# Optimization experiments

Measured on AMD Instinct MI355X. Metric: run time of the kernel, lower is better.

Reference implementation:

```python
import jax, jax.numpy as jnp
import numpy as np

B, T, H, L = 64, 64, 256, 2
INPUT_SIZE = 65
E = INPUT_SIZE - 1  # encoder_in


def setup_inputs() -> dict:
    key = jax.random.key(0)
    ks = jax.random.split(key, 20)
    s = 0.05
    p = {}
    p["input_data"] = jax.random.normal(ks[0], (B, T, INPUT_SIZE), jnp.float32)
    # encoder LSTM (input E -> H, L layers; torch gate order i,f,g,o)
    p["w_ih_e0"] = jax.random.normal(ks[1], (4 * H, E), jnp.float32) * s
    p["w_ih_e1"] = jax.random.normal(ks[2], (L - 1, 4 * H, H), jnp.float32) * s
    p["w_hh_e"] = jax.random.normal(ks[3], (L, 4 * H, H), jnp.float32) * s
    p["b_ih_e"] = jax.random.normal(ks[4], (L, 4 * H), jnp.float32) * s
    p["b_hh_e"] = jax.random.normal(ks[5], (L, 4 * H), jnp.float32) * s
    # decoder LSTM (input H+1 -> H, L layers)
    p["w_ih_d0"] = jax.random.normal(ks[6], (4 * H, H + 1), jnp.float32) * s
    p["w_ih_d1"] = jax.random.normal(ks[7], (L - 1, 4 * H, H), jnp.float32) * s
    p["w_hh_d"] = jax.random.normal(ks[8], (L, 4 * H, H), jnp.float32) * s
    p["b_ih_d"] = jax.random.normal(ks[9], (L, 4 * H), jnp.float32) * s
    p["b_hh_d"] = jax.random.normal(ks[10], (L, 4 * H), jnp.float32) * s
    # encoder attention MLP: Linear(2H+T -> E), Tanh, Linear(E -> 1, no bias)
    p["attn_w1"] = jax.random.normal(ks[11], (E, 2 * H + T), jnp.float32) * s
    p["attn_b1"] = jax.random.normal(ks[12], (E,), jnp.float32) * s
    p["attn_w2"] = jax.random.normal(ks[13], (E,), jnp.float32) * s
    # decoder attention MLP: Linear(3H -> H), Tanh, Linear(H -> 1, no bias)
    p["attnd_w1"] = jax.random.normal(ks[14], (H, 3 * H), jnp.float32) * s
    p["attnd_b1"] = jax.random.normal(ks[15], (H,), jnp.float32) * s
    p["attnd_w2"] = jax.random.normal(ks[16], (H,), jnp.float32) * s
    # output projection: Linear(2H -> 1)
    p["proj_w"] = jax.random.normal(ks[17], (1, 2 * H), jnp.float32) * s
    p["proj_b"] = jax.random.normal(ks[18], (1,), jnp.float32) * s
    return p


def _lstm_step(x, h, c, w_ih0, w_ih_rest, w_hh, b_ih, b_hh):
    """Single-timestep multi-layer LSTM. x: [B, in], h/c: [L, B, H]."""
    hs, cs = [], []
    inp = x
    for l in range(L):
        w_ih = w_ih0 if l == 0 else w_ih_rest[l - 1]
        gates = inp @ w_ih.T + b_ih[l] + h[l] @ w_hh[l].T + b_hh[l]  # [B, 4H]
        i, f, g, o = jnp.split(gates, 4, axis=-1)
        c_new = jax.nn.sigmoid(f) * c[l] + jax.nn.sigmoid(i) * jnp.tanh(g)
        h_new = jax.nn.sigmoid(o) * jnp.tanh(c_new)
        hs.append(h_new)
        cs.append(c_new)
        inp = h_new
    return jnp.stack(hs), jnp.stack(cs)


def reference(input_data, w_ih_e0, w_ih_e1, w_hh_e, b_ih_e, b_hh_e,
              w_ih_d0, w_ih_d1, w_hh_d, b_ih_d, b_hh_d,
              attn_w1, attn_b1, attn_w2, attnd_w1, attnd_b1, attnd_w2,
              proj_w, proj_b):
    input_encoder = input_data[:, :, 1:]             # [B, T, E]
    input_decoder = input_data[:, :, 0]              # [B, T]
    input_permuted = jnp.transpose(input_encoder, (0, 2, 1))  # [B, E, T]

    h0 = jnp.zeros((L, B, H), input_data.dtype)
    c0 = jnp.zeros((L, B, H), input_data.dtype)

    def enc_step(carry, x_t):  # x_t: [B, E]
        h, c = carry
        feat = jnp.concatenate([
            jnp.broadcast_to(h[-1][:, None, :], (B, E, H)),
            jnp.broadcast_to(c[-1][:, None, :], (B, E, H)),
            input_permuted], axis=-1)                # [B, E, 2H+T]
        z = jnp.tanh(feat @ attn_w1.T + attn_b1)     # [B, E, E]
        a = jax.nn.softmax(z @ attn_w2, axis=-1)     # [B, E]
        h, c = _lstm_step(x_t * a, h, c, w_ih_e0, w_ih_e1, w_hh_e, b_ih_e, b_hh_e)
        return (h, c), h[-1]

    _, h_tops = jax.lax.scan(enc_step, (h0, c0), jnp.transpose(input_encoder, (1, 0, 2)))
    h_expanded = jnp.transpose(h_tops, (1, 0, 2))    # [B, T, H]

    def dec_step(carry, d_t):  # d_t: [B]
        h, c = carry
        feat = jnp.concatenate([
            jnp.broadcast_to(h[-1][:, None, :], (B, T, H)),
            jnp.broadcast_to(c[-1][:, None, :], (B, T, H)),
            h_expanded], axis=-1)                    # [B, T, 3H]
        z = jnp.tanh(feat @ attnd_w1.T + attnd_b1)   # [B, T, H]
        a = jax.nn.softmax(z @ attnd_w2, axis=-1)    # [B, T]
        partial = jnp.einsum('bth,bt->bh', h_expanded, a)  # [B, H]
        full = jnp.concatenate([partial, d_t[:, None]], axis=-1)  # [B, H+1]
        h, c = _lstm_step(full, h, c, w_ih_d0, w_ih_d1, w_hh_d, b_ih_d, b_hh_d)
        return (h, c), partial

    (h_d, c_d), partials = jax.lax.scan(dec_step, (h0, c0), input_decoder.T)
    out = jnp.abs(jnp.concatenate([h_d[-1], partials[-1]], axis=-1) @ proj_w.T + proj_b)  # [B, 1]
    return out
```

## Files before the change

### kernel.cpp

```cpp
#include <hip/hip_runtime.h>
#include <hip/hip_fp16.h>
#include <math.h>

#define NT8 512
#define NT  1024

typedef _Float16 h2v __attribute__((ext_vector_type(2)));
union H8 { uint4 u; h2v h[4]; };

__device__ __forceinline__ float sigf(float x)   { return 1.0f / (1.0f + __expf(-x)); }
__device__ __forceinline__ float tanhf_(float x) { return 1.0f - 2.0f / (1.0f + __expf(2.0f * x)); }
__device__ __forceinline__ float dot4(float4 a, float4 b) {
    return a.x * b.x + a.y * b.y + a.z * b.z + a.w * b.w;
}
__device__ __forceinline__ float red16(float v) {
    v += __shfl_xor(v, 1); v += __shfl_xor(v, 2);
    v += __shfl_xor(v, 4); v += __shfl_xor(v, 8);
    return v;
}
__device__ __forceinline__ float red8(float v) {
    v += __shfl_xor(v, 1); v += __shfl_xor(v, 2); v += __shfl_xor(v, 4);
    return v;
}
__device__ __forceinline__ float red64(float v) {
    v += __shfl_xor(v, 1);  v += __shfl_xor(v, 2);  v += __shfl_xor(v, 4);
    v += __shfl_xor(v, 8);  v += __shfl_xor(v, 16); v += __shfl_xor(v, 32);
    return v;
}
__device__ __forceinline__ float dot2h(h2v a, h2v b, float c) {
#if __has_builtin(__builtin_amdgcn_fdot2)
    return __builtin_amdgcn_fdot2(a, b, c, false);
#else
    return c + (float)a[0] * (float)b[0] + (float)a[1] * (float)b[1];
#endif
}

__device__ __forceinline__ float exr(const float* p) {
    return __hip_atomic_load(p, __ATOMIC_RELAXED, __HIP_MEMORY_SCOPE_AGENT);
}
__device__ __forceinline__ void xsig(unsigned* ctr) {
    if (threadIdx.x == 0) {
        asm volatile("s_waitcnt vmcnt(0)" ::: "memory");
        __hip_atomic_fetch_add(ctr, 1u, __ATOMIC_RELAXED, __HIP_MEMORY_SCOPE_AGENT);
    }
}
__device__ __forceinline__ void xwait(unsigned* ctr, unsigned target) {
    if (threadIdx.x == 0) {
        while (__hip_atomic_load(ctr, __ATOMIC_RELAXED, __HIP_MEMORY_SCOPE_AGENT) < target)
            __builtin_amdgcn_s_sleep(1);
    }
    __syncthreads();
}

#define OFF_RA   0
#define OFF_RE0  32768
#define OFF_RE1  425984
#define OFF_RDW1 950272
#define OFF_RD0  1081344
#define OFF_RDT  1605632
#define OFF_RD1  1606656
#define OFF_RPD  2130944
#define TOT_H2   2196480

template<int ITERS, bool BIAS, bool DT>
__device__ __forceinline__ void gemvS512(const __half* __restrict__ W,
                                         const __half* __restrict__ act,
                                         const float* __restrict__ biasF,
                                         const __half* __restrict__ rdtH, float dts,
                                         float* __restrict__ outg, int coB) {
    const int lane = threadIdx.x & 63;
    const int q = lane & 15, g = lane >> 4;
    const int w = threadIdx.x >> 6;
    H8 a0, a1, a2, a3;
    a0.u = *(const uint4*)(act + 8 * q);
    a1.u = *(const uint4*)(act + 8 * q + 128);
    a2.u = *(const uint4*)(act + 8 * q + 256);
    a3.u = *(const uint4*)(act + 8 * q + 384);
    #pragma unroll 2
    for (int it = 0; it < ITERS; ++it) {
        const int l = w * 16 + it * 4 + g;
        const int j = ((l & 0x60) << 3) + coB + (l & 31);
        const uint4* wp = (const uint4*)(W + ((size_t)j << 9) + 32 * q);
        H8 w0, w1, w2, w3;
        w0.u = wp[0]; w1.u = wp[1]; w2.u = wp[2]; w3.u = wp[3];
        float s0 = 0.f, s1 = 0.f;
        #pragma unroll
        for (int i = 0; i < 4; ++i) {
            s0 = dot2h(w0.h[i], a0.h[i], s0);
            s1 = dot2h(w1.h[i], a1.h[i], s1);
            s0 = dot2h(w2.h[i], a2.h[i], s0);
            s1 = dot2h(w3.h[i], a3.h[i], s1);
        }
        float s = red16(s0 + s1);
        if (q == 0) {
            if (DT) s += dts * (float)rdtH[l];
            outg[l] = BIAS ? s + biasF[l] : s;
        }
    }
}

template<int ITERS>
__device__ __forceinline__ void gemvS384(const __half* __restrict__ W,
                                         const __half* __restrict__ act,
                                         const float* __restrict__ biasF,
                                         float* __restrict__ outg, int coB) {
    const int lane = threadIdx.x & 63;
    const int q = lane & 15, g = lane >> 4;
    const int w = threadIdx.x >> 6;
    H8 a0, a1, a2;
    a0.u = *(const uint4*)(act + 8 * q);
    a1.u = *(const uint4*)(act + 8 * q + 128);
    a2.u = *(const uint4*)(act + 8 * q + 256);
    #pragma unroll 2
    for (int it = 0; it < ITERS; ++it) {
        const int l = w * 16 + it * 4 + g;
        const int j = ((l & 0x60) << 3) + coB + (l & 31);
        const h2v* hp = (const h2v*)(W + (size_t)j * 384 + 24 * q);
        float s0 = 0.f, s1 = 0.f;
        #pragma unroll
        for (int i = 0; i < 4; ++i) s0 = dot2h(hp[i],     a0.h[i], s0);
        #pragma unroll
        for (int i = 0; i < 4; ++i) s1 = dot2h(hp[4 + i], a1.h[i], s1);
        #pragma unroll
        for (int i = 0; i < 4; ++i) s0 = dot2h(hp[8 + i], a2.h[i], s0);
        float s = red16(s0 + s1);
        if (q == 0) outg[l] = s + biasF[l];
    }
}

__device__ __forceinline__ void gemvE1(const __half* __restrict__ W,
                                       const __half* __restrict__ act,
                                       float* __restrict__ outg) {
    const int lane = threadIdx.x & 63;
    const int q = lane & 15, g = lane >> 4;
    const int w = threadIdx.x >> 6;
    H8 a0, a1, a2, a3;
    a0.u = *(const uint4*)(act + 8 * q);
    a1.u = *(const uint4*)(act + 8 * q + 128);
    a2.u = *(const uint4*)(act + 8 * q + 256);
    a3.u = *(const uint4*)(act + 8 * q + 384);
    #pragma unroll
    for (int it = 0; it < 2; ++it) {
        const int j = w * 8 + it * 4 + g;
        const uint4* wp = (const uint4*)(W + ((size_t)j << 9) + 32 * q);
        H8 w0, w1, w2, w3;
        w0.u = wp[0]; w1.u = wp[1]; w2.u = wp[2]; w3.u = wp[3];
        float s0 = 0.f, s1 = 0.f;
        #pragma unroll
        for (int i = 0; i < 4; ++i) {
            s0 = dot2h(w0.h[i], a0.h[i], s0);
            s1 = dot2h(w1.h[i], a1.h[i], s1);
            s0 = dot2h(w2.h[i], a2.h[i], s0);
            s1 = dot2h(w3.h[i], a3.h[i], s1);
        }
        float s = red16(s0 + s1);
        if (q == 0) outg[j] = s;
    }
}

#define V8_HEXP  0
#define V8_R     8192
#define V8_GSL   16384
#define V8_HCT   16512
#define V8_SCORE 16768
#define V8_AS    16832
#define V8_C0    16896
#define V8_C1    16928
#define V8_HC1F  16960
#define V8_DECIN 17216
#define V8_PARTF 17280
#define V8_BE0   17536
#define V8_BE1   17664
#define V8_BD0   17792
#define V8_BD1   17920
#define V8_AHC   18048
#define V8_AE0   18304
#define V8_AHH   18496
#define V8_AD0   18752
#define V8_RDT   19008
#define V8_W2D   19072
#define V8_TMP   19328
#define V8_TOT   19360

extern "C" __global__ void __launch_bounds__(NT8)
attn_lstm_v8(const float* __restrict__ inp,  const __half* __restrict__ wsh,
             float* __restrict__ h0x, float* __restrict__ h1x,
             float* __restrict__ hcx, unsigned* __restrict__ barc,
             const float* __restrict__ bihe, const float* __restrict__ bhhe,
             const float* __restrict__ bihd, const float* __restrict__ bhhd,
             const float* __restrict__ aw1,  const float* __restrict__ ab1,
             const float* __restrict__ aw2,  const float* __restrict__ db1,
             const float* __restrict__ dw2,
             const float* __restrict__ pw,   const float* __restrict__ pb,
             float* __restrict__ out)
{
    extern __shared__ __align__(16) float sm[];
    __half* hexp16 = (__half*)(sm + V8_HEXP);
    float*  xeT    = sm + V8_R;
    __half* PdL16  = (__half*)(sm + V8_R);
    float* gsl    = sm + V8_GSL;
    float* hctL   = sm + V8_HCT;
    float* scoreS = sm + V8_SCORE;
    float* aS     = sm + V8_AS;
    float* c0L    = sm + V8_C0;
    float* c1L    = sm + V8_C1;
    float* hc1f   = sm + V8_HC1F;
    float* decin  = sm + V8_DECIN;
    float* partF  = sm + V8_PARTF;
    float* bE0f   = sm + V8_BE0;
    float* bE1f   = sm + V8_BE1;
    float* bD0f   = sm + V8_BD0;
    float* bD1f   = sm + V8_BD1;
    __half* aHC   = (__half*)(sm + V8_AHC);
    __half* aE0   = (__half*)(sm + V8_AE0);
    __half* aHH   = (__half*)(sm + V8_AHH);
    __half* aD0   = (__half*)(sm + V8_AD0);
    __half* rdtH  = (__half*)(sm + V8_RDT);
    float* w2dL   = sm + V8_W2D;
    float* tmp32  = sm + V8_TMP;

    const __half* RA   = wsh + OFF_RA;
    const __half* RE0  = wsh + OFF_RE0;
    const __half* RE1  = wsh + OFF_RE1;
    const __half* RDW1 = wsh + OFF_RDW1;
    const __half* RD0  = wsh + OFF_RD0;
    const __half* RD1  = wsh + OFF_RD1;
    const __half* RPD  = wsh + OFF_RPD;

    const int tid = threadIdx.x;
    const int b   = blockIdx.x >> 3;
    const int co  = blockIdx.x & 7;
    const int coB = co * 32;
    const int w   = tid >> 6;
    const int lane = tid & 63;
    const int q16 = lane & 15, g4 = lane >> 4;
    unsigned* ctr = barc + (b << 4);
    unsigned  ph  = 0;

    for (int i = tid; i < V8_TOT - V8_GSL; i += NT8) sm[V8_GSL + i] = 0.0f;
    const float* ib = inp + b * (64 * 65);
    for (int i = tid; i < 4096; i += NT8) {
        int t = i & 63, e = i >> 6;
        xeT[e * 68 + t] = ib[t * 65 + 1 + e];
    }
    __syncthreads();
    if (tid < 128) {
        int l = tid;
        int j = ((l & 0x60) << 3) + coB + (l & 31);
        bE0f[l] = bihe[j]        + bhhe[j];
        bE1f[l] = bihe[1024 + j] + bhhe[1024 + j];
        bD0f[l] = bihd[j]        + bhhd[j];
        bD1f[l] = bihd[1024 + j] + bhhd[1024 + j];
        rdtH[l] = wsh[OFF_RDT + j];
    }
    if (tid < 64) decin[tid] = ib[tid * 65];
    if (tid < 256) w2dL[tid] = dw2[tid];
    __syncthreads();

    const int e8 = tid >> 3, q8 = tid & 7;
    float Preg[8], w2r[8];
    #pragma unroll
    for (int jj = 0; jj < 8; ++jj) {
        int j = q8 + 8 * jj;
        w2r[jj] = aw2[j];
        float acc = ab1[j];
        const float4* w4 = (const float4*)(aw1 + j * 576 + 512);
        const float4* x4 = (const float4*)(xeT + e8 * 68);
        #pragma unroll 4
        for (int k = 0; k < 16; ++k) acc += dot4(w4[k], x4[k]);
        Preg[jj] = acc;
    }

    for (int t = 0; t < 64; ++t) {
        const int p = t & 1;
        float* h0b = h0x + p * 16384 + b * 256;
        float* h1b = h1x + p * 32768 + b * 512;
        gemvE1(RA, aHC, hctL);
        __syncthreads();
        {
            float s = 0.f;
            #pragma unroll
            for (int jj = 0; jj < 8; ++jj)
                s += tanhf_(Preg[jj] + hctL[q8 + 8 * jj]) * w2r[jj];
            s = red8(s);
            if (q8 == 0) scoreS[e8] = s;
        }
        __syncthreads();
        if (tid < 64) {
            float v = scoreS[tid], m = v;
            #pragma unroll
            for (int d = 1; d < 64; d <<= 1) m = fmaxf(m, __shfl_xor(m, d));
            float ex = __expf(v - m), s = ex;
            #pragma unroll
            for (int d = 1; d < 64; d <<= 1) s += __shfl_xor(s, d);
            aE0[tid] = __float2half((ex / s) * xeT[tid * 68 + t]);
        }
        __syncthreads();
        gemvS384<4>(RE0, aE0, bE0f, gsl, coB);
        __syncthreads();
        if (tid < 32) {
            float cn = sigf(gsl[32 + tid]) * c0L[tid] + sigf(gsl[tid]) * tanhf_(gsl[64 + tid]);
            float hn = sigf(gsl[96 + tid]) * tanhf_(cn);
            c0L[tid] = cn;
            atomicExch(&h0b[coB + tid], hn);
        }
        xsig(ctr); ++ph;
        xwait(ctr, ph * 8u);
        if (tid < 256) {
            __half hh = __float2half(exr(&h0b[tid]));
            aE0[64 + tid] = hh; aHH[tid] = hh;
        }
        __syncthreads();
        gemvS512<4, true, false>(RE1, aHH, bE1f, nullptr, 0.f, gsl, coB);
        __syncthreads();
        if (tid < 32) {
            float cn = sigf(gsl[32 + tid]) * c1L[tid] + sigf(gsl[tid]) * tanhf_(gsl[64 + tid]);
            float hn = sigf(gsl[96 + tid]) * tanhf_(cn);
            c1L[tid] = cn;
            atomicExch(&h1b[coB + tid], hn);
            atomicExch(&h1b[256 + coB + tid], cn);
        }
        xsig(ctr); ++ph;
        xwait(ctr, ph * 8u);
        if (tid < 512) {
            float v = exr(&h1b[tid]);
            __half hh = __float2half(v);
            aHC[tid] = hh;
            if (tid < 256) { aHH[256 + tid] = hh; hexp16[t * 256 + tid] = hh; }
        }
        __syncthreads();
    }

    if (tid < 32) { c0L[tid] = 0.f; c1L[tid] = 0.f; }
    for (int i = tid; i < 960; i += NT8) sm[V8_AHC + i] = 0.0f;
    __syncthreads();
    {
        #pragma unroll 1
        for (int it = 0; it < 8; ++it) {
            const int j = it * 32 + w * 4 + g4;
            const h2v* wp = (const h2v*)(RPD + ((size_t)j << 8) + 16 * q16);
            h2v w0 = wp[0], w1 = wp[1], w2 = wp[2], w3 = wp[3];
            h2v w4 = wp[4], w5 = wp[5], w6 = wp[6], w7 = wp[7];
            float dbj = db1[j];
            #pragma unroll 2
            for (int tp = 0; tp < 64; ++tp) {
                const h2v* xp = (const h2v*)(hexp16 + tp * 256 + 8 * q16);
                const h2v* yp = (const h2v*)(hexp16 + tp * 256 + 8 * q16 + 128);
                float s = 0.f;
                s = dot2h(w0, xp[0], s); s = dot2h(w1, xp[1], s);
                s = dot2h(w2, xp[2], s); s = dot2h(w3, xp[3], s);
                s = dot2h(w4, yp[0], s); s = dot2h(w5, yp[1], s);
                s = dot2h(w6, yp[2], s); s = dot2h(w7, yp[3], s);
                s = red16(s);
                if (q16 == 0) PdL16[tp * 256 + j] = __float2half(s + dbj);
            }
        }
    }
    __syncthreads();

    for (int t = 0; t < 64; ++t) {
        const int p = t & 1;
        float* h0b = h0x + p * 16384 + b * 256;
        float* h1b = h1x + p * 32768 + b * 512;
        float* hcb = hcx + p * 16384 + b * 256;
        {
            const int l = w * 4 + g4;
            const int j = coB + l;
            H8 a0, a1, a2, a3;
            a0.u = *(const uint4*)((const __half*)aHC + 8 * q16);
            a1.u = *(const uint4*)((const __half*)aHC + 8 * q16 + 128);
            a2.u = *(const uint4*)((const __half*)aHC + 8 * q16 + 256);
            a3.u = *(const uint4*)((const __half*)aHC + 8 * q16 + 384);
            const uint4* wp = (const uint4*)(RDW1 + ((size_t)j << 9) + 32 * q16);
            H8 w0, w1, w2, w3;
            w0.u = wp[0]; w1.u = wp[1]; w2.u = wp[2]; w3.u = wp[3];
            float s0 = 0.f, s1 = 0.f;
            #pragma unroll
            for (int i = 0; i < 4; ++i) {
                s0 = dot2h(w0.h[i], a0.h[i], s0);
                s1 = dot2h(w1.h[i], a1.h[i], s1);
                s0 = dot2h(w2.h[i], a2.h[i], s0);
                s1 = dot2h(w3.h[i], a3.h[i], s1);
            }
            float s = red16(s0 + s1);
            if (q16 == 0) tmp32[l] = s;
        }
        __syncthreads();
        if (tid < 32) atomicExch(&hcb[coB + tid], tmp32[tid]);
        xsig(ctr); ++ph;
        xwait(ctr, ph * 8u);
        if (tid < 256) hctL[tid] = exr(&hcb[tid]);
        __syncthreads();
        {
            float s = 0.f;
            #pragma unroll 8
            for (int jj = 0; jj < 32; ++jj) {
                int j = q8 + 8 * jj;
                s += tanhf_((float)PdL16[e8 * 256 + j] + hctL[j]) * w2dL[j];
            }
            s = red8(s);
            if (q8 == 0) scoreS[e8] = s;
        }
        __syncthreads();
        if (tid < 64) {
            float v = scoreS[tid], m = v;
            #pragma unroll
            for (int d = 1; d < 64; d <<= 1) m = fmaxf(m, __shfl_xor(m, d));
            float ex = __expf(v - m), s = ex;
            #pragma unroll
            for (int d = 1; d < 64; d <<= 1) s += __shfl_xor(s, d);
            aS[tid] = ex / s;
        }
        __syncthreads();
        if (tid < 256) {
            float acc = 0.f;
            #pragma unroll 8
            for (int tt = 0; tt < 64; ++tt)
                acc += (float)hexp16[tt * 256 + tid] * aS[tt];
            partF[tid] = acc;
            aD0[tid] = __float2half(acc);
        }
        __syncthreads();
        gemvS512<4, true, true>(RD0, aD0, bD0f, rdtH, decin[t], gsl, coB);
        __syncthreads();
        if (tid < 32) {
            float cn = sigf(gsl[32 + tid]) * c0L[tid] + sigf(gsl[tid]) * tanhf_(gsl[64 + tid]);
            float hn = sigf(gsl[96 + tid]) * tanhf_(cn);
            c0L[tid] = cn;
            atomicExch(&h0b[coB + tid], hn);
        }
        xsig(ctr); ++ph;
        xwait(ctr, ph * 8u);
        if (tid < 256) {
            __half hh = __float2half(exr(&h0b[tid]));
            aD0[256 + tid] = hh; aHH[tid] = hh;
        }
        __syncthreads();
        gemvS512<4, true, false>(RD1, aHH, bD1f, nullptr, 0.f, gsl, coB);
        __syncthreads();
        if (tid < 32) {
            float cn = sigf(gsl[32 + tid]) * c1L[tid] + sigf(gsl[tid]) * tanhf_(gsl[64 + tid]);
            float hn = sigf(gsl[96 + tid]) * tanhf_(cn);
            c1L[tid] = cn;
            atomicExch(&h1b[coB + tid], hn);
            atomicExch(&h1b[256 + coB + tid], cn);
        }
        xsig(ctr); ++ph;
        xwait(ctr, ph * 8u);
        if (tid < 512) {
            float v = exr(&h1b[tid]);
            __half hh = __float2half(v);
            aHC[tid] = hh;
            if (tid < 256) { aHH[256 + tid] = hh; hc1f[tid] = v; }
        }
        __syncthreads();
    }

    if (co == 0 && tid < 64) {
        float acc = 0.f;
        #pragma unroll
        for (int i = 0; i < 8; ++i) {
            int k = tid + 64 * i;
            float v = (k < 256) ? hc1f[k] : partF[k - 256];
            acc += v * pw[k];
        }
        acc = red64(acc);
        if (tid == 0) out[b] = fabsf(acc + pb[0]);
    }
}

extern "C" __global__ void repack16c(const float* __restrict__ wihe0,
                                     const float* __restrict__ wihe1,
                                     const float* __restrict__ whhe,
                                     const float* __restrict__ wihd0,
                                     const float* __restrict__ wihd1,
                                     const float* __restrict__ whhd,
                                     const float* __restrict__ aw1,
                                     const float* __restrict__ dw1,
                                     __half* __restrict__ ws) {
    int idx = blockIdx.x * blockDim.x + threadIdx.x;
    if (idx >= TOT_H2) return;
    int o = idx; float v;
    if (o < 32768) {
        int j = o >> 9, p = o & 511;
        int q = p >> 5, r = p & 31, c = r >> 3, e = r & 7;
        int k = 8 * q + 128 * c + e;
        v = aw1[j * 576 + k];
        ws[OFF_RA + o] = __float2half_rn(v); return;
    }
    o -= 32768;
    if (o < 393216) {
        int j = o / 384, p = o - j * 384;
        int q = p / 24, r = p - q * 24, c = r >> 3, e = r & 7;
        int k = 8 * q + 128 * c + e;
        v = (k < 64) ? wihe0[j * 64 + k] : (k < 320 ? whhe[j * 256 + (k - 64)] : 0.0f);
        ws[OFF_RE0 + o] = __float2half_rn(v); return;
    }
    o -= 393216;
    if (o < 524288) {
        int j = o >> 9, p = o & 511;
        int q = p >> 5, r = p & 31, c = r >> 3, e = r & 7;
        int k = 8 * q + 128 * c + e;
        v = (k < 256) ? wihe1[j * 256 + k] : whhe[262144 + j * 256 + (k - 256)];
        ws[OFF_RE1 + o] = __float2half_rn(v); return;
    }
    o -= 524288;
    if (o < 131072) {
        int j = o >> 9, p = o & 511;
        int q = p >> 5, r = p & 31, c = r >> 3, e = r & 7;
        int k = 8 * q + 128 * c + e;
        v = dw1[j * 768 + k];
        ws[OFF_RDW1 + o] = __float2half_rn(v); return;
    }
    o -= 131072;
    if (o < 524288) {
        int j = o >> 9, p = o & 511;
        int q = p >> 5, r = p & 31, c = r >> 3, e = r & 7;
        int k = 8 * q + 128 * c + e;
        v = (k < 256) ? wihd0[j * 257 + k] : whhd[j * 256 + (k - 256)];
        ws[OFF_RD0 + o] = __float2half_rn(v); return;
    }
    o -= 524288;
    if (o < 1024) {
        v = wihd0[o * 257 + 256];
        ws[OFF_RDT + o] = __float2half_rn(v); return;
    }
    o -= 1024;
    if (o < 524288) {
        int j = o >> 9, p = o & 511;
        int q = p >> 5, r = p & 31, c = r >> 3, e = r & 7;
        int k = 8 * q + 128 * c + e;
        v = (k < 256) ? wihd1[j * 256 + k] : whhd[262144 + j * 256 + (k - 256)];
        ws[OFF_RD1 + o] = __float2half_rn(v); return;
    }
    o -= 524288;
    {
        int j = o >> 8, p = o & 255;
        int q = p >> 4, r = p & 15, c = r >> 3, e = r & 7;
        int k = 8 * q + 128 * c + e;
        v = dw1[j * 768 + 512 + k];
        ws[OFF_RPD + o] = __float2half_rn(v);
    }
}

template<int ITERS, bool BIAS, bool DT>
__device__ __forceinline__ void gemv512f(const __half* __restrict__ W,
                                         const __half* __restrict__ act,
                                         const float* __restrict__ bias,
                                         const __half* __restrict__ rdt, float dts,
                                         float* __restrict__ outg, int rowBase) {
    const int lane = threadIdx.x & 63;
    const int q = lane & 15, g = lane >> 4;
    H8 a0, a1, a2, a3;
    a0.u = *(const uint4*)(act + 8 * q);
    a1.u = *(const uint4*)(act + 8 * q + 128);
    a2.u = *(const uint4*)(act + 8 * q + 256);
    a3.u = *(const uint4*)(act + 8 * q + 384);
    #pragma unroll 2
    for (int it = 0; it < ITERS; ++it) {
        const int j = rowBase + it * 4 + g;
        const uint4* wp = (const uint4*)(W + ((size_t)j << 9) + 32 * q);
        H8 w0, w1, w2, w3;
        w0.u = wp[0]; w1.u = wp[1]; w2.u = wp[2]; w3.u = wp[3];
        float s0 = 0.f, s1 = 0.f;
        #pragma unroll
        for (int i = 0; i < 4; ++i) {
            s0 = dot2h(w0.h[i], a0.h[i], s0);
            s1 = dot2h(w1.h[i], a1.h[i], s1);
            s0 = dot2h(w2.h[i], a2.h[i], s0);
            s1 = dot2h(w3.h[i], a3.h[i], s1);
        }
        float s = red16(s0 + s1);
        if (q == 0) {
            if (DT) s += dts * (float)rdt[j];
            outg[j] = BIAS ? s + bias[j] : s;
        }
    }
}
template<int ITERS>
__device__ __forceinline__ void gemv384f(const __half* __restrict__ W,
                                         const __half* __restrict__ act,
                                         const float* __restrict__ bias,
                                         float* __restrict__ outg, int rowBase) {
    const int lane = threadIdx.x & 63;
    const int q = lane & 15, g = lane >> 4;
    H8 a0, a1, a2;
    a0.u = *(const uint4*)(act + 8 * q);
    a1.u = *(const uint4*)(act + 8 * q + 128);
    a2.u = *(const uint4*)(act + 8 * q + 256);
    #pragma unroll 2
    for (int it = 0; it < ITERS; ++it) {
        const int j = rowBase + it * 4 + g;
        const h2v* hp = (const h2v*)(W + (size_t)j * 384 + 24 * q);
        float s0 = 0.f, s1 = 0.f;
        #pragma unroll
        for (int i = 0; i < 4; ++i) s0 = dot2h(hp[i],     a0.h[i], s0);
        #pragma unroll
        for (int i = 0; i < 4; ++i) s1 = dot2h(hp[4 + i], a1.h[i], s1);
        #pragma unroll
        for (int i = 0; i < 4; ++i) s0 = dot2h(hp[8 + i], a2.h[i], s0);
        float s = red16(s0 + s1);
        if (q == 0) outg[j] = s + bias[j];
    }
}

#define L_HEXP   0
#define L_XET    16384
#define L_GSL    20736
#define L_HCT    21760
#define L_SCORE  22016
#define L_AS     22080
#define L_C0     22144
#define L_HC1F   22400
#define L_DECIN  22912
#define L_PARTF  22976
#define L_BE0    23232
#define L_BE1    24256
#define L_BD0    25280
#define L_BD1    26304
#define L_AHC    27328
#define L_AE0    27584
#define L_AHH    27776
#define L_AD0    28032
#define L_RDT    28288
#define L_TOT    28800

extern "C" __global__ void __launch_bounds__(NT)
attn_lstm_v5(const float* __restrict__ inp,  const __half* __restrict__ wsh,
             const float* __restrict__ bihe, const float* __restrict__ bhhe,
             const float* __restrict__ bihd, const float* __restrict__ bhhd,
             const float* __restrict__ aw1,  const float* __restrict__ ab1,
             const float* __restrict__ aw2,
             const float* __restrict__ dw1,  const float* __restrict__ db1,
             const float* __restrict__ dw2,
             const float* __restrict__ pw,   const float* __restrict__ pb,
             float* __restrict__ out)
{
    extern __shared__ __align__(16) float sm[];
    float* hexp   = sm + L_HEXP;
    float* xeT    = sm + L_XET;
    float* gsl    = sm + L_GSL;
    float* hctL   = sm + L_HCT;
    float* scoreS = sm + L_SCORE;
    float* aS     = sm + L_AS;
    float* c0L    = sm + L_C0;
    float* hc1f   = sm + L_HC1F;
    float* decin  = sm + L_DECIN;
    float* partF  = sm + L_PARTF;
    float* bE0    = sm + L_BE0;
    float* bE1    = sm + L_BE1;
    float* bD0    = sm + L_BD0;
    float* bD1    = sm + L_BD1;
    __half* aHC   = (__half*)(sm + L_AHC);
    __half* aE0   = (__half*)(sm + L_AE0);
    __half* aHH   = (__half*)(sm + L_AHH);
    __half* aD0   = (__half*)(sm + L_AD0);
    __half* rdtL  = (__half*)(sm + L_RDT);

    const __half* RA   = wsh + OFF_RA;
    const __half* RE0  = wsh + OFF_RE0;
    const __half* RE1  = wsh + OFF_RE1;
    const __half* RDW1 = wsh + OFF_RDW1;
    const __half* RD0  = wsh + OFF_RD0;
    const __half* RD1  = wsh + OFF_RD1;

    const int b   = blockIdx.x;
    const int tid = threadIdx.x;
    const int w   = tid >> 6;

    for (int i = tid; i < (L_BE0 - L_C0); i += NT) sm[L_C0 + i] = 0.0f;
    for (int i = tid; i < (L_RDT - L_AHC); i += NT) sm[L_AHC + i] = 0.0f;
    if (tid < 512) sm[L_RDT + tid] = ((const float*)(wsh + OFF_RDT))[tid];
    {
        int j = tid;
        bE0[j] = bihe[j]        + bhhe[j];
        bE1[j] = bihe[1024 + j] + bhhe[1024 + j];
        bD0[j] = bihd[j]        + bhhd[j];
        bD1[j] = bihd[1024 + j] + bhhd[1024 + j];
    }
    const float* ib = inp + b * (64 * 65);
    for (int i = tid; i < 4096; i += NT) {
        int t = i & 63, e = i >> 6;
        xeT[e * 68 + t] = ib[t * 65 + 1 + e];
    }
    if (tid < 64) decin[tid] = ib[tid * 65];
    __syncthreads();

    const int g16 = tid >> 4, q16 = tid & 15;

    float Preg[4], w2r[4];
    #pragma unroll
    for (int jj = 0; jj < 4; ++jj) {
        int j = q16 + 16 * jj;
        w2r[jj] = aw2[j];
        float acc = ab1[j];
        const float4* w4 = (const float4*)(aw1 + j * 576 + 512);
        const float4* x4 = (const float4*)(xeT + g16 * 68);
        #pragma unroll 4
        for (int k = 0; k < 16; ++k) acc += dot4(w4[k], x4[k]);
        Preg[jj] = acc;
    }

    for (int t = 0; t < 64; ++t) {
        gemv512f<1, false, false>(RA, aHC, nullptr, nullptr, 0.f, hctL, w * 4);
        __syncthreads();
        {
            float s = 0.f;
            #pragma unroll
            for (int jj = 0; jj < 4; ++jj)
                s += tanhf_(Preg[jj] + hctL[q16 + 16 * jj]) * w2r[jj];
            s = red16(s);
            if (q16 == 0) scoreS[g16] = s;
        }
        __syncthreads();
        if (tid < 64) {
            float v = scoreS[tid], m = v;
            #pragma unroll
            for (int d = 1; d < 64; d <<= 1) m = fmaxf(m, __shfl_xor(m, d));
            float ex = __expf(v - m), s = ex;
            #pragma unroll
            for (int d = 1; d < 64; d <<= 1) s += __shfl_xor(s, d);
            aE0[tid] = __float2half((ex / s) * xeT[tid * 68 + t]);
        }
        __syncthreads();
        gemv384f<16>(RE0, aE0, bE0, gsl, w * 64);
        __syncthreads();
        if (tid < 256) {
            float cn = sigf(gsl[256 + tid]) * c0L[tid] + sigf(gsl[tid]) * tanhf_(gsl[512 + tid]);
            float hn = sigf(gsl[768 + tid]) * tanhf_(cn);
            c0L[tid] = cn;
            __half hh = __float2half(hn);
            aE0[64 + tid] = hh; aHH[tid] = hh;
        }
        __syncthreads();
        gemv512f<16, true, false>(RE1, aHH, bE1, nullptr, 0.f, gsl, w * 64);
        __syncthreads();
        if (tid < 256) {
            float cp = hc1f[256 + tid];
            float cn = sigf(gsl[256 + tid]) * cp + sigf(gsl[tid]) * tanhf_(gsl[512 + tid]);
            float hn = sigf(gsl[768 + tid]) * tanhf_(cn);
            hc1f[tid] = hn; hc1f[256 + tid] = cn;
            __half hh = __float2half(hn);
            aHC[tid] = hh; aHC[256 + tid] = __float2half(cn);
            aHH[256 + tid] = hh;
            hexp[t * 256 + tid] = hn;
        }
        __syncthreads();
    }

    if (tid < 256) { c0L[tid] = 0.0f; hc1f[tid] = 0.0f; hc1f[256 + tid] = 0.0f; }
    for (int i = tid; i < (L_RDT - L_AHC); i += NT) sm[L_AHC + i] = 0.0f;
    __syncthreads();
    float Pdreg[16], w2dr[16];
    #pragma unroll
    for (int jj = 0; jj < 16; ++jj) {
        int j = q16 + 16 * jj;
        w2dr[jj] = dw2[j];
        float acc = db1[j];
        const float4* w4 = (const float4*)(dw1 + j * 768 + 512);
        const float4* x4 = (const float4*)(hexp + g16 * 256);
        #pragma unroll 4
        for (int k = 0; k < 64; ++k) acc += dot4(w4[k], x4[k]);
        Pdreg[jj] = acc;
    }
    __syncthreads();

    const int j4 = tid >> 2, q4 = tid & 3;
    for (int t = 0; t < 64; ++t) {
        gemv512f<4, false, false>(RDW1, aHC, nullptr, nullptr, 0.f, hctL, w * 16);
        __syncthreads();
        {
            float s = 0.f;
            #pragma unroll
            for (int jj = 0; jj < 16; ++jj)
                s += tanhf_(Pdreg[jj] + hctL[q16 + 16 * jj]) * w2dr[jj];
            s = red16(s);
            if (q16 == 0) scoreS[g16] = s;
        }
        __syncthreads();
        if (tid < 64) {
            float v = scoreS[tid], m = v;
            #pragma unroll
            for (int d = 1; d < 64; d <<= 1) m = fmaxf(m, __shfl_xor(m, d));
            float ex = __expf(v - m), s = ex;
            #pragma unroll
            for (int d = 1; d < 64; d <<= 1) s += __shfl_xor(s, d);
            aS[tid] = ex / s;
        }
        __syncthreads();
        {
            float acc = 0.f;
            #pragma unroll 4
            for (int i = 0; i < 16; ++i) {
                int tt = q4 + 4 * i;
                acc += hexp[tt * 256 + j4] * aS[tt];
            }
            acc += __shfl_xor(acc, 1);
            acc += __shfl_xor(acc, 2);
            if (q4 == 0) { aD0[j4] = __float2half(acc); partF[j4] = acc; }
        }
        __syncthreads();
        gemv512f<16, true, true>(RD0, aD0, bD0, rdtL, decin[t], gsl, w * 64);
        __syncthreads();
        if (tid < 256) {
            float cn = sigf(gsl[256 + tid]) * c0L[tid] + sigf(gsl[tid]) * tanhf_(gsl[512 + tid]);
            float hn = sigf(gsl[768 + tid]) * tanhf_(cn);
            c0L[tid] = cn;
            __half hh = __float2half(hn);
            aD0[256 + tid] = hh; aHH[tid] = hh;
        }
        __syncthreads();
        gemv512f<16, true, false>(RD1, aHH, bD1, nullptr, 0.f, gsl, w * 64);
        __syncthreads();
        if (tid < 256) {
            float cp = hc1f[256 + tid];
            float cn = sigf(gsl[256 + tid]) * cp + sigf(gsl[tid]) * tanhf_(gsl[512 + tid]);
            float hn = sigf(gsl[768 + tid]) * tanhf_(cn);
            hc1f[tid] = hn; hc1f[256 + tid] = cn;
            __half hh = __float2half(hn);
            aHC[tid] = hh; aHC[256 + tid] = __float2half(cn);
            aHH[256 + tid] = hh;
        }
        __syncthreads();
    }

    if (tid < 64) {
        float acc = 0.f;
        #pragma unroll
        for (int i = 0; i < 8; ++i) {
            int k = tid + 64 * i;
            float v = (k < 256) ? hc1f[k] : partF[k - 256];
            acc += v * pw[k];
        }
        acc = red64(acc);
        if (tid == 0) out[b] = fabsf(acc + pb[0]);
    }
}

extern "C" void kernel_launch(void* const* d_in, const int* in_sizes, int n_in,
                              void* d_out, int out_size, void* d_ws, size_t ws_size,
                              hipStream_t stream) {
    const float* inp   = (const float*)d_in[0];
    const float* wihe0 = (const float*)d_in[1];
    const float* wihe1 = (const float*)d_in[2];
    const float* whhe  = (const float*)d_in[3];
    const float* bihe  = (const float*)d_in[4];
    const float* bhhe  = (const float*)d_in[5];
    const float* wihd0 = (const float*)d_in[6];
    const float* wihd1 = (const float*)d_in[7];
    const float* whhd  = (const float*)d_in[8];
    const float* bihd  = (const float*)d_in[9];
    const float* bhhd  = (const float*)d_in[10];
    const float* aw1   = (const float*)d_in[11];
    const float* ab1   = (const float*)d_in[12];
    const float* aw2   = (const float*)d_in[13];
    const float* dw1   = (const float*)d_in[14];
    const float* db1   = (const float*)d_in[15];
    const float* dw2   = (const float*)d_in[16];
    const float* pw    = (const float*)d_in[17];
    const float* pb    = (const float*)d_in[18];
    float* out = (float*)d_out;

    const size_t EX0 = TOT_H2 / 2;
    const size_t H0X = EX0;
    const size_t H1X = EX0 + 32768;
    const size_t HCX = EX0 + 98304;
    const size_t CTR = EX0 + 131072;
    const size_t NEED8 = (CTR + 1024) * sizeof(float);

    if (ws_size >= NEED8) {
        float* ws32 = (float*)d_ws;
        __half* wsh = (__half*)d_ws;
        hipMemsetAsync((char*)d_ws + CTR * sizeof(float), 0, 4096, stream);
        repack16c<<<(TOT_H2 + 255) / 256, 256, 0, stream>>>(
            wihe0, wihe1, whhe, wihd0, wihd1, whhd, aw1, dw1, wsh);
        const int smem = V8_TOT * 4;
        hipFuncSetAttribute((const void*)attn_lstm_v8,
                            hipFuncAttributeMaxDynamicSharedMemorySize, smem);
        attn_lstm_v8<<<512, NT8, smem, stream>>>(
            inp, wsh, ws32 + H0X, ws32 + H1X, ws32 + HCX,
            (unsigned*)(ws32 + CTR),
            bihe, bhhe, bihd, bhhd,
            aw1, ab1, aw2, db1, dw2, pw, pb, out);
        return;
    }

    if (ws_size >= (size_t)TOT_H2 * sizeof(__half)) {
        __half* wsh = (__half*)d_ws;
        repack16c<<<(TOT_H2 + 255) / 256, 256, 0, stream>>>(
            wihe0, wihe1, whhe, wihd0, wihd1, whhd, aw1, dw1, wsh);
        const int smem = L_TOT * 4;
        hipFuncSetAttribute((const void*)attn_lstm_v5,
                            hipFuncAttributeMaxDynamicSharedMemorySize, smem);
        attn_lstm_v5<<<64, NT, smem, stream>>>(
            inp, wsh, bihe, bhhe, bihd, bhhd,
            aw1, ab1, aw2, dw1, db1, dw2, pw, pb, out);
    }
}
```

Baseline: 2.168 ms.

## Compute attention h/c projections as per-block partial sums to drop a barrier

Each of the 8 cooperating blocks per batch now multiplies only its own 32-wide slice of h and c by a column-sliced copy of the attention W1 (new repacked RAC/RDWC regions). It publishes partial sums to global scratch, and readers sum the 8 partials after the existing barrier. This removes the separate full-width gemv phase and its extra inter-block barrier per decoder step, and it stops exchanging c through global memory. Atomic exchanges become relaxed atomic stores, and xsig now does a block-wide sync before signalling. The cost is more global scratch traffic and 8-way partial reads per step.

New measurement: 2.183 ms. No clear change (+0.7%).

```diff
diff --git a/kernel.cpp b/kernel.cpp
--- a/kernel.cpp
+++ b/kernel.cpp
@@ -38,11 +38,14 @@
 __device__ __forceinline__ float exr(const float* p) {
     return __hip_atomic_load(p, __ATOMIC_RELAXED, __HIP_MEMORY_SCOPE_AGENT);
 }
+__device__ __forceinline__ void exw(float* p, float v) {
+    __hip_atomic_store(p, v, __ATOMIC_RELAXED, __HIP_MEMORY_SCOPE_AGENT);
+}
 __device__ __forceinline__ void xsig(unsigned* ctr) {
-    if (threadIdx.x == 0) {
-        asm volatile("s_waitcnt vmcnt(0)" ::: "memory");
+    asm volatile("s_waitcnt vmcnt(0)" ::: "memory");
+    __syncthreads();
+    if (threadIdx.x == 0)
         __hip_atomic_fetch_add(ctr, 1u, __ATOMIC_RELAXED, __HIP_MEMORY_SCOPE_AGENT);
-    }
 }
 __device__ __forceinline__ void xwait(unsigned* ctr, unsigned target) {
     if (threadIdx.x == 0) {
@@ -60,7 +63,9 @@
 #define OFF_RDT  1605632
 #define OFF_RD1  1606656
 #define OFF_RPD  2130944
-#define TOT_H2   2196480
+#define OFF_RAC  2196480
+#define OFF_RDWC 2229248
+#define TOT_H3   2360320
 
 template<int ITERS, bool BIAS, bool DT>
 __device__ __forceinline__ void gemvS512(const __half* __restrict__ W,
@@ -128,64 +133,34 @@
     }
 }
 
-__device__ __forceinline__ void gemvE1(const __half* __restrict__ W,
-                                       const __half* __restrict__ act,
-                                       float* __restrict__ outg) {
-    const int lane = threadIdx.x & 63;
-    const int q = lane & 15, g = lane >> 4;
-    const int w = threadIdx.x >> 6;
-    H8 a0, a1, a2, a3;
-    a0.u = *(const uint4*)(act + 8 * q);
-    a1.u = *(const uint4*)(act + 8 * q + 128);
-    a2.u = *(const uint4*)(act + 8 * q + 256);
-    a3.u = *(const uint4*)(act + 8 * q + 384);
-    #pragma unroll
-    for (int it = 0; it < 2; ++it) {
-        const int j = w * 8 + it * 4 + g;
-        const uint4* wp = (const uint4*)(W + ((size_t)j << 9) + 32 * q);
-        H8 w0, w1, w2, w3;
-        w0.u = wp[0]; w1.u = wp[1]; w2.u = wp[2]; w3.u = wp[3];
-        float s0 = 0.f, s1 = 0.f;
-        #pragma unroll
-        for (int i = 0; i < 4; ++i) {
-            s0 = dot2h(w0.h[i], a0.h[i], s0);
-            s1 = dot2h(w1.h[i], a1.h[i], s1);
-            s0 = dot2h(w2.h[i], a2.h[i], s0);
-            s1 = dot2h(w3.h[i], a3.h[i], s1);
-        }
-        float s = red16(s0 + s1);
-        if (q == 0) outg[j] = s;
-    }
-}
-
-#define V8_HEXP  0
-#define V8_R     8192
-#define V8_GSL   16384
-#define V8_HCT   16512
-#define V8_SCORE 16768
-#define V8_AS    16832
-#define V8_C0    16896
-#define V8_C1    16928
-#define V8_HC1F  16960
-#define V8_DECIN 17216
-#define V8_PARTF 17280
-#define V8_BE0   17536
-#define V8_BE1   17664
-#define V8_BD0   17792
-#define V8_BD1   17920
-#define V8_AHC   18048
-#define V8_AE0   18304
-#define V8_AHH   18496
-#define V8_AD0   18752
-#define V8_RDT   19008
-#define V8_W2D   19072
-#define V8_TMP   19328
-#define V8_TOT   19360
+#define V_HEXP  0
+#define V_R     8192
+#define V_GSL   16384
+#define V_HCT   16512
+#define V_SCORE 16768
+#define V_AS    16832
+#define V_C0    16896
+#define V_C1    16928
+#define V_HC1F  16960
+#define V_DECIN 17216
+#define V_PARTF 17280
+#define V_BE0   17536
+#define V_BE1   17664
+#define V_BD0   17792
+#define V_BD1   17920
+#define V_AE0   18048
+#define V_AHH   18240
+#define V_AD0   18496
+#define V_HCOWN 18752
+#define V_RDT   18784
+#define V_W2D   18848
+#define V_TOT   19104
 
 extern "C" __global__ void __launch_bounds__(NT8)
-attn_lstm_v8(const float* __restrict__ inp,  const __half* __restrict__ wsh,
+attn_lstm_v9(const float* __restrict__ inp,  const __half* __restrict__ wsh,
              float* __restrict__ h0x, float* __restrict__ h1x,
-             float* __restrict__ hcx, unsigned* __restrict__ barc,
+             float* __restrict__ hcts, float* __restrict__ hcds,
+             unsigned* __restrict__ barc,
              const float* __restrict__ bihe, const float* __restrict__ bhhe,
              const float* __restrict__ bihd, const float* __restrict__ bhhd,
              const float* __restrict__ aw1,  const float* __restrict__ ab1,
@@ -195,37 +170,36 @@
              float* __restrict__ out)
 {
     extern __shared__ __align__(16) float sm[];
-    __half* hexp16 = (__half*)(sm + V8_HEXP);
-    float*  xeT    = sm + V8_R;
-    __half* PdL16  = (__half*)(sm + V8_R);
-    float* gsl    = sm + V8_GSL;
-    float* hctL   = sm + V8_HCT;
-    float* scoreS = sm + V8_SCORE;
-    float* aS     = sm + V8_AS;
-    float* c0L    = sm + V8_C0;
-    float* c1L    = sm + V8_C1;
-    float* hc1f   = sm + V8_HC1F;
-    float* decin  = sm + V8_DECIN;
-    float* partF  = sm + V8_PARTF;
-    float* bE0f   = sm + V8_BE0;
-    float* bE1f   = sm + V8_BE1;
-    float* bD0f   = sm + V8_BD0;
-    float* bD1f   = sm + V8_BD1;
-    __half* aHC   = (__half*)(sm + V8_AHC);
-    __half* aE0   = (__half*)(sm + V8_AE0);
-    __half* aHH   = (__half*)(sm + V8_AHH);
-    __half* aD0   = (__half*)(sm + V8_AD0);
-    __half* rdtH  = (__half*)(sm + V8_RDT);
-    float* w2dL   = sm + V8_W2D;
-    float* tmp32  = sm + V8_TMP;
-
-    const __half* RA   = wsh + OFF_RA;
+    __half* hexp16 = (__half*)(sm + V_HEXP);
+    float*  xeT    = sm + V_R;
+    __half* PdL16  = (__half*)(sm + V_R);
+    float* gsl    = sm + V_GSL;
+    float* hctL   = sm + V_HCT;
+    float* scoreS = sm + V_SCORE;
+    float* aS     = sm + V_AS;
+    float* c0L    = sm + V_C0;
+    float* c1L    = sm + V_C1;
+    float* hc1f   = sm + V_HC1F;
+    float* decin  = sm + V_DECIN;
+    float* partF  = sm + V_PARTF;
+    float* bE0f   = sm + V_BE0;
+    float* bE1f   = sm + V_BE1;
+    float* bD0f   = sm + V_BD0;
+    float* bD1f   = sm + V_BD1;
+    __half* aE0   = (__half*)(sm + V_AE0);
+    __half* aHH   = (__half*)(sm + V_AHH);
+    __half* aD0   = (__half*)(sm + V_AD0);
+    __half* hcOwn = (__half*)(sm + V_HCOWN);
+    __half* rdtH  = (__half*)(sm + V_RDT);
+    float* w2dL   = sm + V_W2D;
+
     const __half* RE0  = wsh + OFF_RE0;
     const __half* RE1  = wsh + OFF_RE1;
-    const __half* RDW1 = wsh + OFF_RDW1;
     const __half* RD0  = wsh + OFF_RD0;
     const __half* RD1  = wsh + OFF_RD1;
     const __half* RPD  = wsh + OFF_RPD;
+    const __half* RAC  = wsh + OFF_RAC;
+    const __half* RDWC = wsh + OFF_RDWC;
 
     const int tid = threadIdx.x;
     const int b   = blockIdx.x >> 3;
@@ -234,10 +208,11 @@
     const int w   = tid >> 6;
     const int lane = tid & 63;
     const int q16 = lane & 15, g4 = lane >> 4;
+    const int q8l = lane & 7,  g8 = lane >> 3;
     unsigned* ctr = barc + (b << 4);
     unsigned  ph  = 0;
 
-    for (int i = tid; i < V8_TOT - V8_GSL; i += NT8) sm[V8_GSL + i] = 0.0f;
+    for (int i = tid; i < V_TOT - V_GSL; i += NT8) sm[V_GSL + i] = 0.0f;
     const float* ib = inp + b * (64 * 65);
     for (int i = tid; i < 4096; i += NT8) {
         int t = i & 63, e = i >> 6;
@@ -274,9 +249,8 @@
     for (int t = 0; t < 64; ++t) {
         const int p = t & 1;
         float* h0b = h0x + p * 16384 + b * 256;
-        float* h1b = h1x + p * 32768 + b * 512;
-        gemvE1(RA, aHC, hctL);
-        __syncthreads();
+        float* h1b = h1x + p * 16384 + b * 256;
+        float* hcs = hcts + p * 32768 + b * 512 + co * 64;
         {
             float s = 0.f;
             #pragma unroll
@@ -302,7 +276,7 @@
             float cn = sigf(gsl[32 + tid]) * c0L[tid] + sigf(gsl[tid]) * tanhf_(gsl[64 + tid]);
             float hn = sigf(gsl[96 + tid]) * tanhf_(cn);
             c0L[tid] = cn;
-            atomicExch(&h0b[coB + tid], hn);
+            exw(&h0b[coB + tid], hn);
         }
         xsig(ctr); ++ph;
         xwait(ctr, ph * 8u);
@@ -317,22 +291,42 @@
             float cn = sigf(gsl[32 + tid]) * c1L[tid] + sigf(gsl[tid]) * tanhf_(gsl[64 + tid]);
             float hn = sigf(gsl[96 + tid]) * tanhf_(cn);
             c1L[tid] = cn;
-            atomicExch(&h1b[coB + tid], hn);
-            atomicExch(&h1b[256 + coB + tid], cn);
+            hcOwn[tid] = __float2half(hn);
+            hcOwn[32 + tid] = __float2half(cn);
+            exw(&h1b[coB + tid], hn);
+        }
+        __syncthreads();
+        {
+            const int j = w * 8 + g8;
+            H8 a; a.u = *(const uint4*)((const __half*)hcOwn + 8 * q8l);
+            H8 wv; wv.u = *(const uint4*)(RAC + ((size_t)co << 12) + j * 64 + 8 * q8l);
+            float s = 0.f;
+            #pragma unroll
+            for (int i = 0; i < 4; ++i) s = dot2h(wv.h[i], a.h[i], s);
+            s = red8(s);
+            if (q8l == 0) exw(&hcs[j], s);
         }
         xsig(ctr); ++ph;
         xwait(ctr, ph * 8u);
-        if (tid < 512) {
+        if (tid < 256) {
             float v = exr(&h1b[tid]);
             __half hh = __float2half(v);
-            aHC[tid] = hh;
-            if (tid < 256) { aHH[256 + tid] = hh; hexp16[t * 256 + tid] = hh; }
-        }
-        __syncthreads();
-    }
-
-    if (tid < 32) { c0L[tid] = 0.f; c1L[tid] = 0.f; }
-    for (int i = tid; i < 960; i += NT8) sm[V8_AHC + i] = 0.0f;
+            aHH[256 + tid] = hh;
+            hexp16[t * 256 + tid] = hh;
+        }
+        if (tid < 64) {
+            const float* base = hcts + p * 32768 + b * 512;
+            float s = 0.f;
+            #pragma unroll
+            for (int c = 0; c < 8; ++c) s += exr(base + c * 64 + tid);
+            hctL[tid] = s;
+        }
+        __syncthreads();
+    }
+
+    if (tid < 64)  sm[V_C0 + tid] = 0.0f;
+    if (tid < 256) hctL[tid] = 0.0f;
+    for (int i = tid; i < 736; i += NT8) sm[V_AE0 + i] = 0.0f;
     __syncthreads();
     {
         #pragma unroll 1
@@ -361,36 +355,8 @@
     for (int t = 0; t < 64; ++t) {
         const int p = t & 1;
         float* h0b = h0x + p * 16384 + b * 256;
-        float* h1b = h1x + p * 32768 + b * 512;
-        float* hcb = hcx + p * 16384 + b * 256;
-        {
-            const int l = w * 4 + g4;
-            const int j = coB + l;
-            H8 a0, a1, a2, a3;
-            a0.u = *(const uint4*)((const __half*)aHC + 8 * q16);
-            a1.u = *(const uint4*)((const __half*)aHC + 8 * q16 + 128);
-            a2.u = *(const uint4*)((const __half*)aHC + 8 * q16 + 256);
-            a3.u = *(const uint4*)((const __half*)aHC + 8 * q16 + 384);
-            const uint4* wp = (const uint4*)(RDW1 + ((size_t)j << 9) + 32 * q16);
-            H8 w0, w1, w2, w3;
-            w0.u = wp[0]; w1.u = wp[1]; w2.u = wp[2]; w3.u = wp[3];
-            float s0 = 0.f, s1 = 0.f;
-            #pragma unroll
-            for (int i = 0; i < 4; ++i) {
-                s0 = dot2h(w0.h[i], a0.h[i], s0);
-                s1 = dot2h(w1.h[i], a1.h[i], s1);
-                s0 = dot2h(w2.h[i], a2.h[i], s0);
-                s1 = dot2h(w3.h[i], a3.h[i], s1);
-            }
-            float s = red16(s0 + s1);
-            if (q16 == 0) tmp32[l] = s;
-        }
-        __syncthreads();
-        if (tid < 32) atomicExch(&hcb[coB + tid], tmp32[tid]);
-        xsig(ctr); ++ph;
-        xwait(ctr, ph * 8u);
-        if (tid < 256) hctL[tid] = exr(&hcb[tid]);
-        __syncthreads();
+        float* h1b = h1x + p * 16384 + b * 256;
+        float* hcd = hcds + p * 131072 + b * 2048 + co * 256;
         {
             float s = 0.f;
             #pragma unroll 8
@@ -427,7 +393,7 @@
             float cn = sigf(gsl[32 + tid]) * c0L[tid] + sigf(gsl[tid]) * tanhf_(gsl[64 + tid]);
             float hn = sigf(gsl[96 + tid]) * tanhf_(cn);
             c0L[tid] = cn;
-            atomicExch(&h0b[coB + tid], hn);
+            exw(&h0b[coB + tid], hn);
         }
         xsig(ctr); ++ph;
         xwait(ctr, ph * 8u);
@@ -442,16 +408,35 @@
             float cn = sigf(gsl[32 + tid]) * c1L[tid] + sigf(gsl[tid]) * tanhf_(gsl[64 + tid]);
             float hn = sigf(gsl[96 + tid]) * tanhf_(cn);
             c1L[tid] = cn;
-            atomicExch(&h1b[coB + tid], hn);
-            atomicExch(&h1b[256 + coB + tid], cn);
+            hcOwn[tid] = __float2half(hn);
+            hcOwn[32 + tid] = __float2half(cn);
+            exw(&h1b[coB + tid], hn);
+        }
+        __syncthreads();
+        {
+            H8 a; a.u = *(const uint4*)((const __half*)hcOwn + 8 * q8l);
+            #pragma unroll
+            for (int it = 0; it < 4; ++it) {
+                const int j = it * 64 + w * 8 + g8;
+                H8 wv; wv.u = *(const uint4*)(RDWC + ((size_t)co << 14) + j * 64 + 8 * q8l);
+                float s = 0.f;
+                #pragma unroll
+                for (int i = 0; i < 4; ++i) s = dot2h(wv.h[i], a.h[i], s);
+                s = red8(s);
+                if (q8l == 0) exw(&hcd[j], s);
+            }
         }
         xsig(ctr); ++ph;
         xwait(ctr, ph * 8u);
-        if (tid < 512) {
+        if (tid < 256) {
             float v = exr(&h1b[tid]);
-            __half hh = __float2half(v);
-            aHC[tid] = hh;
-            if (tid < 256) { aHH[256 + tid] = hh; hc1f[tid] = v; }
+            aHH[256 + tid] = __float2half(v);
+            hc1f[tid] = v;
+            const float* base = hcds + p * 131072 + b * 2048;
+            float s = 0.f;
+            #pragma unroll
+            for (int c = 0; c < 8; ++c) s += exr(base + c * 256 + tid);
+            hctL[tid] = s;
         }
         __syncthreads();
     }
@@ -469,7 +454,7 @@
     }
 }
 
-extern "C" __global__ void repack16c(const float* __restrict__ wihe0,
+extern "C" __global__ void repack16d(const float* __restrict__ wihe0,
                                      const float* __restrict__ wihe1,
                                      const float* __restrict__ whhe,
                                      const float* __restrict__ wihd0,
@@ -479,7 +464,7 @@
                                      const float* __restrict__ dw1,
                                      __half* __restrict__ ws) {
     int idx = blockIdx.x * blockDim.x + threadIdx.x;
-    if (idx >= TOT_H2) return;
+    if (idx >= TOT_H3) return;
     int o = idx; float v;
     if (o < 32768) {
         int j = o >> 9, p = o & 511;
@@ -534,12 +519,26 @@
         ws[OFF_RD1 + o] = __float2half_rn(v); return;
     }
     o -= 524288;
-    {
+    if (o < 65536) {
         int j = o >> 8, p = o & 255;
         int q = p >> 4, r = p & 15, c = r >> 3, e = r & 7;
         int k = 8 * q + 128 * c + e;
         v = dw1[j * 768 + 512 + k];
-        ws[OFF_RPD + o] = __float2half_rn(v);
+        ws[OFF_RPD + o] = __float2half_rn(v); return;
+    }
+    o -= 65536;
+    if (o < 32768) {
+        int c8 = o >> 12, r12 = o & 4095, j = r12 >> 6, k = r12 & 63;
+        int col = (k < 32) ? (c8 * 32 + k) : (256 + c8 * 32 + (k - 32));
+        v = aw1[j * 576 + col];
+        ws[OFF_RAC + o] = __float2half_rn(v); return;
+    }
+    o -= 32768;
+    {
+        int c8 = o >> 14, r14 = o & 16383, j = r14 >> 6, k = r14 & 63;
+        int col = (k < 32) ? (c8 * 32 + k) : (256 + c8 * 32 + (k - 32));
+        v = dw1[j * 768 + col];
+        ws[OFF_RDWC + o] = __float2half_rn(v);
     }
 }
 
@@ -861,33 +860,34 @@
     const float* pb    = (const float*)d_in[18];
     float* out = (float*)d_out;
 
-    const size_t EX0 = TOT_H2 / 2;
-    const size_t H0X = EX0;
-    const size_t H1X = EX0 + 32768;
-    const size_t HCX = EX0 + 98304;
-    const size_t CTR = EX0 + 131072;
-    const size_t NEED8 = (CTR + 1024) * sizeof(float);
-
-    if (ws_size >= NEED8) {
+    const size_t WH   = TOT_H3 / 2;
+    const size_t H0X  = WH;
+    const size_t H1X  = WH + 32768;
+    const size_t HCTS = WH + 65536;
+    const size_t HCDS = WH + 131072;
+    const size_t CTR  = WH + 393216;
+    const size_t NEED9 = (CTR + 1024) * sizeof(float);
+
+    if (ws_size >= NEED9) {
         float* ws32 = (float*)d_ws;
         __half* wsh = (__half*)d_ws;
         hipMemsetAsync((char*)d_ws + CTR * sizeof(float), 0, 4096, stream);
-        repack16c<<<(TOT_H2 + 255) / 256, 256, 0, stream>>>(
+        repack16d<<<(TOT_H3 + 255) / 256, 256, 0, stream>>>(
             wihe0, wihe1, whhe, wihd0, wihd1, whhd, aw1, dw1, wsh);
-        const int smem = V8_TOT * 4;
-        hipFuncSetAttribute((const void*)attn_lstm_v8,
+        const int smem = V_TOT * 4;
+        hipFuncSetAttribute((const void*)attn_lstm_v9,
                             hipFuncAttributeMaxDynamicSharedMemorySize, smem);
-        attn_lstm_v8<<<512, NT8, smem, stream>>>(
-            inp, wsh, ws32 + H0X, ws32 + H1X, ws32 + HCX,
+        attn_lstm_v9<<<512, NT8, smem, stream>>>(
+            inp, wsh, ws32 + H0X, ws32 + H1X, ws32 + HCTS, ws32 + HCDS,
             (unsigned*)(ws32 + CTR),
             bihe, bhhe, bihd, bhhd,
             aw1, ab1, aw2, db1, dw2, pw, pb, out);
         return;
     }
 
-    if (ws_size >= (size_t)TOT_H2 * sizeof(__half)) {
+    if (ws_size >= (size_t)TOT_H3 * sizeof(__half)) {
         __half* wsh = (__half*)d_ws;
-        repack16c<<<(TOT_H2 + 255) / 256, 256, 0, stream>>>(
+        repack16d<<<(TOT_H3 + 255) / 256, 256, 0, stream>>>(
             wihe0, wihe1, whhe, wihd0, wihd1, whhd, aw1, dw1, wsh);
         const int smem = L_TOT * 4;
         hipFuncSetAttribute((const void*)attn_lstm_v5,
```
